# Performance work log

Measured on AMD Instinct MI355X. Metric: run time of the kernel, lower is better.

The kernel has to match this reference:

```python
import jax, jax.numpy as jnp
import numpy as np

N = 100000
E = 300000
IN_C = 256
HID = 256   # 2 * out_channels
OUT_C = 128


def setup_inputs() -> dict:
    key = jax.random.key(0)
    k1, k2, k3, k4, k5 = jax.random.split(key, 5)
    x = jax.random.normal(k1, (N, IN_C), dtype=jnp.float32)
    edge_index = jax.random.randint(k2, (2, E), 0, N, dtype=jnp.int64)
    # Glorot-style init scale for GEMM weights
    W1 = jax.random.normal(k3, (IN_C, HID), dtype=jnp.float32) * (1.0 / np.sqrt(IN_C))
    b1 = jnp.zeros((HID,), dtype=jnp.float32)
    W2 = jax.random.normal(k4, (HID, OUT_C), dtype=jnp.float32) * (1.0 / np.sqrt(HID))
    b2 = jnp.zeros((OUT_C,), dtype=jnp.float32)
    return {"x": x, "edge_index": edge_index, "W1": W1, "b1": b1, "W2": W2, "b2": b2}


def _gcn_conv(x, W, b, src, dst, norm, n_nodes):
    # x: [N, Fin] -> transform then gather-scale-scatter aggregate
    h = x @ W                                   # [N, Fout]
    msgs = h[src] * norm[:, None]               # [E+N, Fout] (includes self-loops)
    out = jax.ops.segment_sum(msgs, dst, num_segments=n_nodes)
    return out + b


def _gcn_norm(edge_index, n_nodes):
    # add self-loops, compute symmetric deg^-1/2 normalization (PyG GCNConv default)
    loops = jnp.arange(n_nodes, dtype=edge_index.dtype)
    src = jnp.concatenate([edge_index[0], loops])
    dst = jnp.concatenate([edge_index[1], loops])
    deg = jax.ops.segment_sum(jnp.ones_like(dst, dtype=jnp.float32), dst, num_segments=n_nodes)
    dinv = jnp.where(deg > 0, jax.lax.rsqrt(deg), 0.0)
    norm = dinv[src] * dinv[dst]                # [E+N]
    return src, dst, norm


def reference(x, edge_index, W1, b1, W2, b2):
    n_nodes = x.shape[0]
    src, dst, norm = _gcn_norm(edge_index, n_nodes)
    h = _gcn_conv(x, W1, b1, src, dst, norm, n_nodes)
    h = jax.nn.relu(h)
    # dropout is identity in eval mode (reference baseline runs deterministic eval)
    return _gcn_conv(h, W2, b2, src, dst, norm, n_nodes)
```

## Files before the change

### kernel.cpp

```cpp
#include <hip/hip_runtime.h>
#include <stdint.h>

#define IN_C  256
#define HID   256
#define OUT_C 128
#define SCAN_BS 1024

typedef __bf16 bf16x8 __attribute__((ext_vector_type(8)));
typedef float  f32x4  __attribute__((ext_vector_type(4)));
typedef unsigned short u16x8 __attribute__((ext_vector_type(8)));
typedef unsigned short u16x4 __attribute__((ext_vector_type(4)));
typedef unsigned short u16x2 __attribute__((ext_vector_type(2)));

static __device__ __forceinline__ unsigned short f2b(float f) {
    union { float f; uint32_t u; } v; v.f = f;
    uint32_t r = v.u + 0x7fffu + ((v.u >> 16) & 1u);
    return (unsigned short)(r >> 16);
}
static __device__ __forceinline__ float b2f(unsigned short b) {
    union { uint32_t u; float f; } v; v.u = ((uint32_t)b) << 16;
    return v.f;
}

__global__ void k_zero_i(int* __restrict__ p, int n) {
    int i = blockIdx.x * blockDim.x + threadIdx.x;
    if (i < n) p[i] = 0;
}

__global__ void k_count(const int* __restrict__ dst, int* __restrict__ cnt, int e) {
    int i = blockIdx.x * blockDim.x + threadIdx.x;
    if (i < e) atomicAdd(&cnt[dst[i]], 1);
}

__global__ __launch_bounds__(SCAN_BS) void k_scan_block(
    const int* __restrict__ cnt, int* __restrict__ rs, int* __restrict__ bsum, int n) {
    __shared__ int s[SCAN_BS];
    const int tid = threadIdx.x;
    const int i = blockIdx.x * SCAN_BS + tid;
    int v = (i < n) ? cnt[i] : 0;
    s[tid] = v;
    __syncthreads();
    for (int off = 1; off < SCAN_BS; off <<= 1) {
        int t = (tid >= off) ? s[tid - off] : 0;
        __syncthreads();
        s[tid] += t;
        __syncthreads();
    }
    if (i < n) rs[i] = s[tid] - v;
    if (tid == SCAN_BS - 1) bsum[blockIdx.x] = s[tid];
}

__global__ void k_scan_sums(int* __restrict__ bsum, int nb) {
    __shared__ int s[128];
    const int tid = threadIdx.x;
    int v = (tid < nb) ? bsum[tid] : 0;
    s[tid] = v;
    __syncthreads();
    for (int off = 1; off < 128; off <<= 1) {
        int t = (tid >= off) ? s[tid - off] : 0;
        __syncthreads();
        s[tid] += t;
        __syncthreads();
    }
    if (tid < nb) bsum[tid] = s[tid] - v;
}

__global__ void k_scan_add(int* __restrict__ rs, int* __restrict__ cur,
                           const int* __restrict__ bsum, const int* __restrict__ cnt,
                           float* __restrict__ dinv, int n) {
    int i = blockIdx.x * blockDim.x + threadIdx.x;
    if (i < n) {
        int v = rs[i] + bsum[i >> 10];
        rs[i] = v;
        cur[i] = v;
        dinv[i] = rsqrtf((float)(cnt[i] + 1));
    }
}

__global__ void k_fill(const int* __restrict__ src, const int* __restrict__ dst,
                       int* __restrict__ cur, int* __restrict__ csr, int e) {
    int i = blockIdx.x * blockDim.x + threadIdx.x;
    if (i < e) {
        int p = atomicAdd(&cur[dst[i]], 1);
        csr[p] = src[i];
    }
}

__global__ void k_prep(const float* __restrict__ W1, const float* __restrict__ W2,
                       unsigned short* __restrict__ W1T, unsigned short* __restrict__ W2T) {
    int i = blockIdx.x * blockDim.x + threadIdx.x;
    if (i < 65536) W1T[i] = f2b(W1[(i & 255) * HID + (i >> 8)]);
    if (i < 32768) W2T[i] = f2b(W2[(i & 255) * OUT_C + (i >> 8)]);
}

__global__ __launch_bounds__(512) void k_gemm1(
    const float* __restrict__ x, const unsigned short* __restrict__ W1T,
    unsigned short* __restrict__ t1, int n) {
    __shared__ __align__(16) unsigned short As[128 * 64];
    __shared__ __align__(16) unsigned short Bs[256 * 64];
    const int tid  = threadIdx.x;
    const int row0 = blockIdx.x * 128;
    const int wid = tid >> 6, lane = tid & 63;
    const int wm = wid >> 2, wn = wid & 3;
    const int lrow = lane & 15, lgrp = lane >> 4;

    f32x4 acc[4][4];
    #pragma unroll
    for (int i = 0; i < 4; ++i)
        #pragma unroll
        for (int j = 0; j < 4; ++j)
            acc[i][j] = (f32x4){0.f, 0.f, 0.f, 0.f};

    for (int kt = 0; kt < 4; ++kt) {
        #pragma unroll
        for (int i = 0; i < 2; ++i) {
            int chunk = tid + 512 * i;
            int r = chunk >> 3, c = chunk & 7;
            int grow = row0 + r;
            u16x8 pk = {0, 0, 0, 0, 0, 0, 0, 0};
            if (grow < n) {
                const float* sp = x + (size_t)grow * IN_C + kt * 64 + c * 8;
                float4 a = *(const float4*)sp;
                float4 b = *(const float4*)(sp + 4);
                pk[0] = f2b(a.x); pk[1] = f2b(a.y); pk[2] = f2b(a.z); pk[3] = f2b(a.w);
                pk[4] = f2b(b.x); pk[5] = f2b(b.y); pk[6] = f2b(b.z); pk[7] = f2b(b.w);
            }
            *(u16x8*)&As[r * 64 + ((c ^ (r & 7)) * 8)] = pk;
        }
        #pragma unroll
        for (int i = 0; i < 4; ++i) {
            int chunk = tid + 512 * i;
            int nn = chunk >> 3, c = chunk & 7;
            u16x8 pk = *(const u16x8*)&W1T[(size_t)nn * 256 + kt * 64 + c * 8];
            *(u16x8*)&Bs[nn * 64 + ((c ^ (nn & 7)) * 8)] = pk;
        }
        __syncthreads();
        #pragma unroll
        for (int kk = 0; kk < 2; ++kk) {
            const int cfrag = kk * 4 + lgrp;
            bf16x8 av[4], bv[4];
            #pragma unroll
            for (int mf = 0; mf < 4; ++mf) {
                int r = wm * 64 + mf * 16 + lrow;
                av[mf] = *(const bf16x8*)&As[r * 64 + ((cfrag ^ (r & 7)) * 8)];
            }
            #pragma unroll
            for (int nf = 0; nf < 4; ++nf) {
                int cc = wn * 64 + nf * 16 + lrow;
                bv[nf] = *(const bf16x8*)&Bs[cc * 64 + ((cfrag ^ (cc & 7)) * 8)];
            }
            #pragma unroll
            for (int mf = 0; mf < 4; ++mf)
                #pragma unroll
                for (int nf = 0; nf < 4; ++nf)
                    acc[mf][nf] = __builtin_amdgcn_mfma_f32_16x16x32_bf16(
                        av[mf], bv[nf], acc[mf][nf], 0, 0, 0);
        }
        __syncthreads();
    }
    #pragma unroll
    for (int mf = 0; mf < 4; ++mf)
        #pragma unroll
        for (int j = 0; j < 4; ++j) {
            int grow = row0 + wm * 64 + mf * 16 + lgrp * 4 + j;
            if (grow < n) {
                #pragma unroll
                for (int nf = 0; nf < 4; ++nf) {
                    int col = wn * 64 + nf * 16 + lrow;
                    t1[(size_t)grow * HID + col] = f2b(acc[mf][nf][j]);
                }
            }
        }
}

__global__ __launch_bounds__(256) void k_agg1(
    const unsigned short* __restrict__ t1, const float* __restrict__ dinv,
    const int* __restrict__ rs, const int* __restrict__ cnt,
    const int* __restrict__ csr, const float* __restrict__ b1,
    unsigned short* __restrict__ out1, int n) {
    const int node = blockIdx.x * 4 + (threadIdx.x >> 6);
    if (node >= n) return;
    const int lane = threadIdx.x & 63;
    const float di = dinv[node];
    u16x4 v = *(const u16x4*)&t1[(size_t)node * HID + lane * 4];
    const float w0 = di * di;
    float a0 = b2f(v[0]) * w0, a1 = b2f(v[1]) * w0, a2 = b2f(v[2]) * w0, a3 = b2f(v[3]) * w0;
    const int beg = rs[node], m = cnt[node];
    for (int j = 0; j < m; ++j) {
        int s = csr[beg + j];
        float w = dinv[s] * di;
        u16x4 u = *(const u16x4*)&t1[(size_t)s * HID + lane * 4];
        a0 += b2f(u[0]) * w; a1 += b2f(u[1]) * w; a2 += b2f(u[2]) * w; a3 += b2f(u[3]) * w;
    }
    float4 bb = *(const float4*)(b1 + lane * 4);
    u16x4 o;
    o[0] = f2b(fmaxf(a0 + bb.x, 0.f));
    o[1] = f2b(fmaxf(a1 + bb.y, 0.f));
    o[2] = f2b(fmaxf(a2 + bb.z, 0.f));
    o[3] = f2b(fmaxf(a3 + bb.w, 0.f));
    *(u16x4*)&out1[(size_t)node * HID + lane * 4] = o;
}

__global__ __launch_bounds__(256) void k_gemm2(
    const unsigned short* __restrict__ out1, const unsigned short* __restrict__ W2T,
    unsigned short* __restrict__ t2, int n) {
    __shared__ __align__(16) unsigned short As[128 * 64];
    __shared__ __align__(16) unsigned short Bs[128 * 64];
    const int tid  = threadIdx.x;
    const int row0 = blockIdx.x * 128;
    const int wid = tid >> 6, lane = tid & 63;
    const int wm = wid >> 1, wn = wid & 1;
    const int lrow = lane & 15, lgrp = lane >> 4;

    f32x4 acc[4][4];
    #pragma unroll
    for (int i = 0; i < 4; ++i)
        #pragma unroll
        for (int j = 0; j < 4; ++j)
            acc[i][j] = (f32x4){0.f, 0.f, 0.f, 0.f};

    for (int kt = 0; kt < 4; ++kt) {
        #pragma unroll
        for (int i = 0; i < 4; ++i) {
            int chunk = tid + 256 * i;
            int r = chunk >> 3, c = chunk & 7;
            int grow = row0 + r;
            u16x8 pk = {0, 0, 0, 0, 0, 0, 0, 0};
            if (grow < n)
                pk = *(const u16x8*)&out1[(size_t)grow * HID + kt * 64 + c * 8];
            *(u16x8*)&As[r * 64 + ((c ^ (r & 7)) * 8)] = pk;
        }
        #pragma unroll
        for (int i = 0; i < 4; ++i) {
            int chunk = tid + 256 * i;
            int nn = chunk >> 3, c = chunk & 7;
            u16x8 pk = *(const u16x8*)&W2T[(size_t)nn * 256 + kt * 64 + c * 8];
            *(u16x8*)&Bs[nn * 64 + ((c ^ (nn & 7)) * 8)] = pk;
        }
        __syncthreads();
        #pragma unroll
        for (int kk = 0; kk < 2; ++kk) {
            const int cfrag = kk * 4 + lgrp;
            bf16x8 av[4], bv[4];
            #pragma unroll
            for (int mf = 0; mf < 4; ++mf) {
                int r = wm * 64 + mf * 16 + lrow;
                av[mf] = *(const bf16x8*)&As[r * 64 + ((cfrag ^ (r & 7)) * 8)];
            }
            #pragma unroll
            for (int nf = 0; nf < 4; ++nf) {
                int cc = wn * 64 + nf * 16 + lrow;
                bv[nf] = *(const bf16x8*)&Bs[cc * 64 + ((cfrag ^ (cc & 7)) * 8)];
            }
            #pragma unroll
            for (int mf = 0; mf < 4; ++mf)
                #pragma unroll
                for (int nf = 0; nf < 4; ++nf)
                    acc[mf][nf] = __builtin_amdgcn_mfma_f32_16x16x32_bf16(
                        av[mf], bv[nf], acc[mf][nf], 0, 0, 0);
        }
        __syncthreads();
    }
    #pragma unroll
    for (int mf = 0; mf < 4; ++mf)
        #pragma unroll
        for (int j = 0; j < 4; ++j) {
            int grow = row0 + wm * 64 + mf * 16 + lgrp * 4 + j;
            if (grow < n) {
                #pragma unroll
                for (int nf = 0; nf < 4; ++nf) {
                    int col = wn * 64 + nf * 16 + lrow;
                    t2[(size_t)grow * OUT_C + col] = f2b(acc[mf][nf][j]);
                }
            }
        }
}

__global__ __launch_bounds__(256) void k_agg2(
    const unsigned short* __restrict__ t2, const float* __restrict__ dinv,
    const int* __restrict__ rs, const int* __restrict__ cnt,
    const int* __restrict__ csr, const float* __restrict__ b2,
    float* __restrict__ out, int n) {
    const int node = blockIdx.x * 4 + (threadIdx.x >> 6);
    if (node >= n) return;
    const int lane = threadIdx.x & 63;
    const float di = dinv[node];
    u16x2 v = *(const u16x2*)&t2[(size_t)node * OUT_C + lane * 2];
    const float w0 = di * di;
    float a0 = b2f(v[0]) * w0, a1 = b2f(v[1]) * w0;
    const int beg = rs[node], m = cnt[node];
    for (int j = 0; j < m; ++j) {
        int s = csr[beg + j];
        float w = dinv[s] * di;
        u16x2 u = *(const u16x2*)&t2[(size_t)s * OUT_C + lane * 2];
        a0 += b2f(u[0]) * w; a1 += b2f(u[1]) * w;
    }
    float2 bb = *(const float2*)(b2 + lane * 2);
    float2 o = {a0 + bb.x, a1 + bb.y};
    *(float2*)&out[(size_t)node * OUT_C + lane * 2] = o;
}

extern "C" void kernel_launch(void* const* d_in, const int* in_sizes, int n_in,
                              void* d_out, int out_size, void* d_ws, size_t ws_size,
                              hipStream_t stream) {
    const float* x  = (const float*)d_in[0];
    const int*   ei = (const int*)d_in[1];
    const float* W1 = (const float*)d_in[2];
    const float* b1 = (const float*)d_in[3];
    const float* W2 = (const float*)d_in[4];
    const float* b2 = (const float*)d_in[5];
    float* out = (float*)d_out;

    const int n = in_sizes[0] / IN_C;
    const int e = in_sizes[1] / 2;
    const int* src = ei;
    const int* dst = ei + e;

    int*   cnt  = (int*)d_ws;
    int*   rs   = cnt + n;
    int*   cur  = rs + n;
    int*   bsum = cur + n;
    int*   csr  = bsum + 128;
    float* dinv = (float*)(csr + e);
    unsigned short* W1T = (unsigned short*)(dinv + n);
    unsigned short* W2T = W1T + 65536;
    unsigned short* t1  = W2T + 32768;
    unsigned short* out1 = t1 + (size_t)n * HID;
    unsigned short* t2  = t1;

    const int nb = (n + SCAN_BS - 1) / SCAN_BS;

    k_zero_i<<<(n + 255) / 256, 256, 0, stream>>>(cnt, n);
    k_count<<<(e + 255) / 256, 256, 0, stream>>>(dst, cnt, e);
    k_scan_block<<<nb, SCAN_BS, 0, stream>>>(cnt, rs, bsum, n);
    k_scan_sums<<<1, 128, 0, stream>>>(bsum, nb);
    k_scan_add<<<(n + 255) / 256, 256, 0, stream>>>(rs, cur, bsum, cnt, dinv, n);
    k_fill<<<(e + 255) / 256, 256, 0, stream>>>(src, dst, cur, csr, e);
    k_prep<<<256, 256, 0, stream>>>(W1, W2, W1T, W2T);

    const int mb = (n + 127) / 128;
    k_gemm1<<<mb, 512, 0, stream>>>(x, W1T, t1, n);
    k_agg1<<<(n + 3) / 4, 256, 0, stream>>>(t1, dinv, rs, cnt, csr, b1, out1, n);
    k_gemm2<<<mb, 256, 0, stream>>>(out1, W2T, t2, n);
    k_agg2<<<(n + 3) / 4, 256, 0, stream>>>(t2, dinv, rs, cnt, csr, b2, out, n);
}
```

Before: 225.4 us.

## Precompute edge weights into CSR pairs and aggregate two nodes per wavefront

The CSR array now stores (source, normalized weight) pairs, with the self-loop inserted as the first entry of each row, so the aggregation kernels no longer gather dinv[src] for every edge. Each wavefront now processes two destination nodes in an interleaved loop, which gives more independent memory loads in flight and half as many blocks. The cost is a larger CSR (8 bytes per entry), extra work in the fill kernel, and divergence when the two nodes have different degrees.

```diff
diff --git a/kernel.cpp b/kernel.cpp
--- a/kernel.cpp
+++ b/kernel.cpp
@@ -37,7 +37,7 @@
     __shared__ int s[SCAN_BS];
     const int tid = threadIdx.x;
     const int i = blockIdx.x * SCAN_BS + tid;
-    int v = (i < n) ? cnt[i] : 0;
+    int v = (i < n) ? cnt[i] + 1 : 0;
     s[tid] = v;
     __syncthreads();
     for (int off = 1; off < SCAN_BS; off <<= 1) {
@@ -67,22 +67,26 @@
 
 __global__ void k_scan_add(int* __restrict__ rs, int* __restrict__ cur,
                            const int* __restrict__ bsum, const int* __restrict__ cnt,
-                           float* __restrict__ dinv, int n) {
+                           float* __restrict__ dinv, int2* __restrict__ csrw, int n) {
     int i = blockIdx.x * blockDim.x + threadIdx.x;
     if (i < n) {
         int v = rs[i] + bsum[i >> 10];
         rs[i] = v;
-        cur[i] = v;
-        dinv[i] = rsqrtf((float)(cnt[i] + 1));
+        cur[i] = v + 1;
+        float dp1 = (float)(cnt[i] + 1);
+        dinv[i] = rsqrtf(dp1);
+        csrw[v] = make_int2(i, __float_as_int(1.0f / dp1));
     }
 }
 
 __global__ void k_fill(const int* __restrict__ src, const int* __restrict__ dst,
-                       int* __restrict__ cur, int* __restrict__ csr, int e) {
+                       const float* __restrict__ dinv,
+                       int* __restrict__ cur, int2* __restrict__ csrw, int e) {
     int i = blockIdx.x * blockDim.x + threadIdx.x;
     if (i < e) {
-        int p = atomicAdd(&cur[dst[i]], 1);
-        csr[p] = src[i];
+        int s = src[i], d = dst[i];
+        int p = atomicAdd(&cur[d], 1);
+        csrw[p] = make_int2(s, __float_as_int(dinv[s] * dinv[d]));
     }
 }
 
@@ -174,31 +178,52 @@
 }
 
 __global__ __launch_bounds__(256) void k_agg1(
-    const unsigned short* __restrict__ t1, const float* __restrict__ dinv,
-    const int* __restrict__ rs, const int* __restrict__ cnt,
-    const int* __restrict__ csr, const float* __restrict__ b1,
-    unsigned short* __restrict__ out1, int n) {
-    const int node = blockIdx.x * 4 + (threadIdx.x >> 6);
-    if (node >= n) return;
+    const unsigned short* __restrict__ t1, const int* __restrict__ rs,
+    const int* __restrict__ cnt, const int2* __restrict__ csrw,
+    const float* __restrict__ b1, unsigned short* __restrict__ out1, int n) {
+    const int w = blockIdx.x * 4 + (threadIdx.x >> 6);
+    const int nodeA = w * 2, nodeB = w * 2 + 1;
+    if (nodeA >= n) return;
+    const bool hasB = (nodeB < n);
     const int lane = threadIdx.x & 63;
-    const float di = dinv[node];
-    u16x4 v = *(const u16x4*)&t1[(size_t)node * HID + lane * 4];
-    const float w0 = di * di;
-    float a0 = b2f(v[0]) * w0, a1 = b2f(v[1]) * w0, a2 = b2f(v[2]) * w0, a3 = b2f(v[3]) * w0;
-    const int beg = rs[node], m = cnt[node];
-    for (int j = 0; j < m; ++j) {
-        int s = csr[beg + j];
-        float w = dinv[s] * di;
-        u16x4 u = *(const u16x4*)&t1[(size_t)s * HID + lane * 4];
-        a0 += b2f(u[0]) * w; a1 += b2f(u[1]) * w; a2 += b2f(u[2]) * w; a3 += b2f(u[3]) * w;
-    }
-    float4 bb = *(const float4*)(b1 + lane * 4);
+    const int ch = lane * 4;
+    const int begA = rs[nodeA], mA = cnt[nodeA] + 1;
+    int begB = 0, mB = 0;
+    if (hasB) { begB = rs[nodeB]; mB = cnt[nodeB] + 1; }
+    float a0 = 0.f, a1 = 0.f, a2 = 0.f, a3 = 0.f;
+    float c0 = 0.f, c1 = 0.f, c2 = 0.f, c3 = 0.f;
+    const int mmax = mA > mB ? mA : mB;
+    for (int j = 0; j < mmax; ++j) {
+        if (j < mA) {
+            int2 p = csrw[begA + j];
+            float wA = __int_as_float(p.y);
+            u16x4 u = *(const u16x4*)&t1[(size_t)p.x * HID + ch];
+            a0 += b2f(u[0]) * wA; a1 += b2f(u[1]) * wA;
+            a2 += b2f(u[2]) * wA; a3 += b2f(u[3]) * wA;
+        }
+        if (j < mB) {
+            int2 p = csrw[begB + j];
+            float wB = __int_as_float(p.y);
+            u16x4 u = *(const u16x4*)&t1[(size_t)p.x * HID + ch];
+            c0 += b2f(u[0]) * wB; c1 += b2f(u[1]) * wB;
+            c2 += b2f(u[2]) * wB; c3 += b2f(u[3]) * wB;
+        }
+    }
+    float4 bb = *(const float4*)(b1 + ch);
     u16x4 o;
     o[0] = f2b(fmaxf(a0 + bb.x, 0.f));
     o[1] = f2b(fmaxf(a1 + bb.y, 0.f));
     o[2] = f2b(fmaxf(a2 + bb.z, 0.f));
     o[3] = f2b(fmaxf(a3 + bb.w, 0.f));
-    *(u16x4*)&out1[(size_t)node * HID + lane * 4] = o;
+    *(u16x4*)&out1[(size_t)nodeA * HID + ch] = o;
+    if (hasB) {
+        u16x4 q;
+        q[0] = f2b(fmaxf(c0 + bb.x, 0.f));
+        q[1] = f2b(fmaxf(c1 + bb.y, 0.f));
+        q[2] = f2b(fmaxf(c2 + bb.z, 0.f));
+        q[3] = f2b(fmaxf(c3 + bb.w, 0.f));
+        *(u16x4*)&out1[(size_t)nodeB * HID + ch] = q;
+    }
 }
 
 __global__ __launch_bounds__(256) void k_gemm2(
@@ -277,27 +302,38 @@
 }
 
 __global__ __launch_bounds__(256) void k_agg2(
-    const unsigned short* __restrict__ t2, const float* __restrict__ dinv,
-    const int* __restrict__ rs, const int* __restrict__ cnt,
-    const int* __restrict__ csr, const float* __restrict__ b2,
-    float* __restrict__ out, int n) {
-    const int node = blockIdx.x * 4 + (threadIdx.x >> 6);
-    if (node >= n) return;
+    const unsigned short* __restrict__ t2, const int* __restrict__ rs,
+    const int* __restrict__ cnt, const int2* __restrict__ csrw,
+    const float* __restrict__ b2, float* __restrict__ out, int n) {
+    const int w = blockIdx.x * 4 + (threadIdx.x >> 6);
+    const int nodeA = w * 2, nodeB = w * 2 + 1;
+    if (nodeA >= n) return;
+    const bool hasB = (nodeB < n);
     const int lane = threadIdx.x & 63;
-    const float di = dinv[node];
-    u16x2 v = *(const u16x2*)&t2[(size_t)node * OUT_C + lane * 2];
-    const float w0 = di * di;
-    float a0 = b2f(v[0]) * w0, a1 = b2f(v[1]) * w0;
-    const int beg = rs[node], m = cnt[node];
-    for (int j = 0; j < m; ++j) {
-        int s = csr[beg + j];
-        float w = dinv[s] * di;
-        u16x2 u = *(const u16x2*)&t2[(size_t)s * OUT_C + lane * 2];
-        a0 += b2f(u[0]) * w; a1 += b2f(u[1]) * w;
-    }
-    float2 bb = *(const float2*)(b2 + lane * 2);
-    float2 o = {a0 + bb.x, a1 + bb.y};
-    *(float2*)&out[(size_t)node * OUT_C + lane * 2] = o;
+    const int ch = lane * 2;
+    const int begA = rs[nodeA], mA = cnt[nodeA] + 1;
+    int begB = 0, mB = 0;
+    if (hasB) { begB = rs[nodeB]; mB = cnt[nodeB] + 1; }
+    float a0 = 0.f, a1 = 0.f, c0 = 0.f, c1 = 0.f;
+    const int mmax = mA > mB ? mA : mB;
+    for (int j = 0; j < mmax; ++j) {
+        if (j < mA) {
+            int2 p = csrw[begA + j];
+            float wA = __int_as_float(p.y);
+            u16x2 u = *(const u16x2*)&t2[(size_t)p.x * OUT_C + ch];
+            a0 += b2f(u[0]) * wA; a1 += b2f(u[1]) * wA;
+        }
+        if (j < mB) {
+            int2 p = csrw[begB + j];
+            float wB = __int_as_float(p.y);
+            u16x2 u = *(const u16x2*)&t2[(size_t)p.x * OUT_C + ch];
+            c0 += b2f(u[0]) * wB; c1 += b2f(u[1]) * wB;
+        }
+    }
+    float2 bb = *(const float2*)(b2 + ch);
+    *(float2*)&out[(size_t)nodeA * OUT_C + ch] = make_float2(a0 + bb.x, a1 + bb.y);
+    if (hasB)
+        *(float2*)&out[(size_t)nodeB * OUT_C + ch] = make_float2(c0 + bb.x, c1 + bb.y);
 }
 
 extern "C" void kernel_launch(void* const* d_in, const int* in_sizes, int n_in,
@@ -320,9 +356,9 @@
     int*   rs   = cnt + n;
     int*   cur  = rs + n;
     int*   bsum = cur + n;
-    int*   csr  = bsum + 128;
-    float* dinv = (float*)(csr + e);
-    unsigned short* W1T = (unsigned short*)(dinv + n);
+    float* dinv = (float*)(bsum + 128);
+    int2*  csrw = (int2*)(dinv + n);
+    unsigned short* W1T = (unsigned short*)(csrw + (size_t)e + n);
     unsigned short* W2T = W1T + 65536;
     unsigned short* t1  = W2T + 32768;
     unsigned short* out1 = t1 + (size_t)n * HID;
@@ -334,13 +370,14 @@
     k_count<<<(e + 255) / 256, 256, 0, stream>>>(dst, cnt, e);
     k_scan_block<<<nb, SCAN_BS, 0, stream>>>(cnt, rs, bsum, n);
     k_scan_sums<<<1, 128, 0, stream>>>(bsum, nb);
-    k_scan_add<<<(n + 255) / 256, 256, 0, stream>>>(rs, cur, bsum, cnt, dinv, n);
-    k_fill<<<(e + 255) / 256, 256, 0, stream>>>(src, dst, cur, csr, e);
+    k_scan_add<<<(n + 255) / 256, 256, 0, stream>>>(rs, cur, bsum, cnt, dinv, csrw, n);
+    k_fill<<<(e + 255) / 256, 256, 0, stream>>>(src, dst, dinv, cur, csrw, e);
     k_prep<<<256, 256, 0, stream>>>(W1, W2, W1T, W2T);
 
     const int mb = (n + 127) / 128;
     k_gemm1<<<mb, 512, 0, stream>>>(x, W1T, t1, n);
-    k_agg1<<<(n + 3) / 4, 256, 0, stream>>>(t1, dinv, rs, cnt, csr, b1, out1, n);
+    const int aggblk = (n + 7) / 8;
+    k_agg1<<<aggblk, 256, 0, stream>>>(t1, rs, cnt, csrw, b1, out1, n);
     k_gemm2<<<mb, 256, 0, stream>>>(out1, W2T, t2, n);
-    k_agg2<<<(n + 3) / 4, 256, 0, stream>>>(t2, dinv, rs, cnt, csr, b2, out, n);
-}
+    k_agg2<<<aggblk, 256, 0, stream>>>(t2, rs, cnt, csrw, b2, out, n);
+}
```

Result: faster. 213.8 us (-5.1%).
